# Optimization experiments

Measured on AMD Instinct MI355X. Metric: run time of the kernel, lower is better.

The kernel has to match this reference:

```python
import jax, jax.numpy as jnp
import numpy as np

B, S, D, E, K = 4, 4096, 4096, 64, 8


def setup_inputs() -> dict:
    key = jax.random.key(0)
    k1, k2, k3, k4 = jax.random.split(key, 4)
    scale = 1.0 / np.sqrt(D)
    return {
        "mh_output": jax.random.normal(k1, (B, S, D), dtype=jnp.float32),
        "W_route": jax.random.normal(k2, (E, D), dtype=jnp.float32) * scale,
        "b_route": jnp.zeros((E,), dtype=jnp.float32),
        "W_noise": jax.random.normal(k3, (E, D), dtype=jnp.float32) * scale,
        "b_noise": jnp.zeros((E,), dtype=jnp.float32),
        "noise_eps": jax.random.normal(k4, (B, S, E), dtype=jnp.float32),
        "top_k": K,
    }


def reference(mh_output, W_route, b_route, W_noise, b_noise, noise_eps, top_k):
    # two skinny GEMMs: [B,S,D] x [D,E] -> [B,S,E]
    logits = jnp.einsum("bsd,ed->bse", mh_output, W_route) + b_route
    noise_logits = jnp.einsum("bsd,ed->bse", mh_output, W_noise) + b_noise
    noisy_logits = logits + noise_eps * jax.nn.softplus(noise_logits)
    # top-k selection per token over the expert dim
    _, indices = jax.lax.top_k(noisy_logits, top_k)  # [B,S,K]
    # scatter top-k logits into a -inf tensor == mask non-topk entries
    mask = jnp.any(jax.nn.one_hot(indices, noisy_logits.shape[-1], dtype=jnp.bool_), axis=-2)  # [B,S,E]
    sparse_logits = jnp.where(mask, noisy_logits, -jnp.inf)
    router_output = jax.nn.softmax(sparse_logits, axis=-1)
    return router_output, indices
```

## Files before the change

### kernel.cpp

```cpp
#include <hip/hip_runtime.h>
#include <math.h>

#define D_DIM 4096
#define E_DIM 64
#define KTOP 8
#define TAU 2e-4f
#define BM 64
#define NTS 64
#define STB 49152
#define NST 3

#define WS_LIST 1024
#define WS_IMG 66560
#define WS_Z   (WS_IMG + 2097152)

typedef __attribute__((ext_vector_type(8))) short bf16x8;
typedef __attribute__((ext_vector_type(4))) float f32x4;

#define MFMA(a, b, c) __builtin_amdgcn_mfma_f32_16x16x32_bf16(a, b, c, 0, 0, 0)

typedef const __attribute__((address_space(1))) void gas_void;
typedef __attribute__((address_space(3))) void las_void;
#define GLL16(src, dst) \
    __builtin_amdgcn_global_load_lds((gas_void*)(src), (las_void*)(dst), 16, 0, 0)
#define SCHED_FENCE() __builtin_amdgcn_sched_barrier(0)

__device__ inline void split8(float4 p, float4 q, bf16x8& h8, bf16x8& l8) {
    float xx[8] = {p.x, p.y, p.z, p.w, q.x, q.y, q.z, q.w};
    union { unsigned int w[4]; bf16x8 v; } H, L;
    #pragma unroll
    for (int i = 0; i < 4; ++i) {
        float a = xx[2 * i], b = xx[2 * i + 1];
        unsigned int hw;
        asm("v_cvt_pk_bf16_f32 %0, %1, %2" : "=v"(hw) : "v"(a), "v"(b));
        float ha = __uint_as_float(hw << 16);
        float hb = __uint_as_float(hw & 0xFFFF0000u);
        float ra = a - ha, rb = b - hb;
        unsigned int lw;
        asm("v_cvt_pk_bf16_f32 %0, %1, %2" : "=v"(lw) : "v"(ra), "v"(rb));
        H.w[i] = hw; L.w[i] = lw;
    }
    h8 = H.v; l8 = L.v;
}

__global__ __launch_bounds__(256)
void preconv(const float* __restrict__ Wr, const float* __restrict__ Wn,
             unsigned short* __restrict__ img, unsigned int* __restrict__ cnt)
{
    if (blockIdx.x == 0 && threadIdx.x == 0) *cnt = 0u;
    int t = blockIdx.x * 256 + threadIdx.x;
    int kt = t >> 9, rem = t & 511;
    int koff = rem >> 7, col = rem & 127;
    int k = kt * 32 + koff * 8;
    const float* base = (col < E_DIM) ? (Wr + (size_t)col * D_DIM)
                                      : (Wn + (size_t)(col - E_DIM) * D_DIM);
    float4 x0 = *(const float4*)(base + k);
    float4 x1 = *(const float4*)(base + k + 4);
    bf16x8 h8, l8;
    split8(x0, x1, h8, l8);
    size_t o = (size_t)kt * 8192 + koff * 1024 + col * 8;
    *(bf16x8*)(img + o) = h8;
    *(bf16x8*)(img + o + 4096) = l8;
}

__global__ __launch_bounds__(512)
void gemm_k(const float* __restrict__ mh,
            const unsigned short* __restrict__ Wimg,
            float* __restrict__ zbuf)
{
    extern __shared__ char smem[];

    const int tid  = threadIdx.x;
    const int lane = tid & 63;
    const int wv   = tid >> 6;
    const int wr   = wv >> 1;
    const int wc   = wv & 1;
    const int tok0 = blockIdx.x * BM;
    const int rloc = lane & 15;
    const int koff = lane >> 4;
    const int row  = wr * 16 + rloc;
    const int rsw  = row & 15;

    int boff[4];
    #pragma unroll
    for (int fc = 0; fc < 4; ++fc)
        boff[fc] = koff * 1024 + (wc * 64 + fc * 16 + rloc) * 8;

    const int4* gimg = (const int4*)Wimg;

    const int a_tok = tid >> 4;
    const int a_kq  = (tid & 15) ^ (a_tok & 15);
    const float* asrc0 = mh + (size_t)(tok0 + a_tok) * D_DIM + a_kq * 4;
    const float* asrc1 = mh + (size_t)(tok0 + a_tok + 32) * D_DIM + a_kq * 4;

    f32x4 acc[4];
    #pragma unroll
    for (int fc = 0; fc < 4; ++fc) acc[fc] = {0.f, 0.f, 0.f, 0.f};

    auto stage_issue = [&](int t) {
        char* sb = smem + (t % NST) * STB;
        const int4* gB = gimg + (size_t)t * 2048 + tid;
        int4* dB = (int4*)sb + tid;
        GLL16(gB, dB);
        GLL16(gB + 512,  dB + 512);
        GLL16(gB + 1024, dB + 1024);
        GLL16(gB + 1536, dB + 1536);
        int4* dA = (int4*)(sb + 32768) + tid;
        GLL16(asrc0 + t * 64, dA);
        GLL16(asrc1 + t * 64, dA + 512);
    };

    stage_issue(0);
    SCHED_FENCE();
    stage_issue(1);
    SCHED_FENCE();
    asm volatile("s_waitcnt vmcnt(6)" ::: "memory");
    SCHED_FENCE();
    __builtin_amdgcn_s_barrier();
    SCHED_FENCE();

    for (int kt = 0; kt < NTS; ++kt) {
        if (kt + 2 < NTS) stage_issue(kt + 2);
        SCHED_FENCE();
        {
            const char* sb = smem + (kt % NST) * STB;
            const unsigned short* Bst = (const unsigned short*)sb;
            const char* sa = sb + 32768;
            #pragma unroll
            for (int s = 0; s < 2; ++s) {
                const int kf = s * 8 + 2 * koff;
                float4 f0 = *(const float4*)(sa + (row * 16 + ((kf)     ^ rsw)) * 16);
                float4 f1 = *(const float4*)(sa + (row * 16 + ((kf + 1) ^ rsw)) * 16);
                bf16x8 ah, al;
                split8(f0, f1, ah, al);
                const unsigned short* bb = Bst + s * 8192;
                #pragma unroll
                for (int fc = 0; fc < 4; ++fc) {
                    bf16x8 bh = *(const bf16x8*)(bb + boff[fc]);
                    bf16x8 bl = *(const bf16x8*)(bb + 4096 + boff[fc]);
                    acc[fc] = MFMA(ah, bh, acc[fc]);
                    acc[fc] = MFMA(al, bh, acc[fc]);
                    acc[fc] = MFMA(ah, bl, acc[fc]);
                }
            }
        }
        SCHED_FENCE();
        if (kt + 2 < NTS) {
            asm volatile("s_waitcnt vmcnt(6) lgkmcnt(0)" ::: "memory");
        } else {
            asm volatile("s_waitcnt vmcnt(0) lgkmcnt(0)" ::: "memory");
        }
        SCHED_FENCE();
        __builtin_amdgcn_s_barrier();
        SCHED_FENCE();
    }

    float* zb = zbuf + (size_t)tok0 * 128;
    #pragma unroll
    for (int fc = 0; fc < 4; ++fc) {
        const int col = wc * 64 + fc * 16 + rloc;
        #pragma unroll
        for (int rg = 0; rg < 4; ++rg) {
            const int r = wr * 16 + koff * 4 + rg;
            zb[r * 128 + col] = acc[fc][rg];
        }
    }
}

__global__ __launch_bounds__(256)
void epi_k(const float* __restrict__ zbuf,
           const float* __restrict__ br, const float* __restrict__ bn,
           const float* __restrict__ eps,
           float* __restrict__ out_probs, float* __restrict__ out_idx,
           unsigned int* __restrict__ cnt, int* __restrict__ list)
{
    __shared__ float zs[32 * 132];
    const int tid  = threadIdx.x;
    const int lane = tid & 63;
    const int wv   = tid >> 6;
    const int tok0 = blockIdx.x * 32;

    for (int i = tid; i < 1024; i += 256) {
        int t = i >> 5, q = i & 31;
        float4 v = *(const float4*)(zbuf + (size_t)(tok0 + t) * 128 + q * 4);
        int b = t * 132 + q * 4;
        zs[b] = v.x; zs[b + 1] = v.y; zs[b + 2] = v.z; zs[b + 3] = v.w;
    }
    __syncthreads();

    {
        const int t  = tid >> 3;
        const int e0 = (tid & 7) << 3;
        const float* ep = eps + (size_t)(tok0 + t) * E_DIM + e0;
        #pragma unroll
        for (int j = 0; j < 8; ++j) {
            float zr = zs[t * 132 + e0 + j] + br[e0 + j];
            float zn = zs[t * 132 + 64 + e0 + j] + bn[e0 + j];
            float sp = fmaxf(zn, 0.f) + log1pf(expf(-fabsf(zn)));
            zs[t * 132 + e0 + j] = zr + ep[j] * sp;
        }
    }
    __syncthreads();

    for (int tk = 0; tk < 8; ++tk) {
        int t = wv * 8 + tk;
        float v0 = zs[t * 132 + lane];
        float v  = v0;
        float m0 = 0.f, denom = 0.f, prev = 0.f, mingap = INFINITY;
        bool selected = false;
        int rankedIdx = 0;
        #pragma unroll
        for (int k = 0; k < KTOP + 1; ++k) {
            float mv = v; int mi = lane;
            #pragma unroll
            for (int off = 32; off > 0; off >>= 1) {
                float ov = __shfl_xor(mv, off);
                int   oi = __shfl_xor(mi, off);
                if (ov > mv || (ov == mv && oi < mi)) { mv = ov; mi = oi; }
            }
            if (k == 0) m0 = mv; else mingap = fminf(mingap, prev - mv);
            prev = mv;
            if (k < KTOP) {
                denom += expf(mv - m0);
                if (lane == mi) { selected = true; v = -INFINITY; }
                if (lane == k) rankedIdx = mi;
            }
        }
        float p = selected ? expf(v0 - m0) / denom : 0.f;
        size_t tg = (size_t)(tok0 + t);
        out_probs[tg * E_DIM + lane] = p;
        if (lane < KTOP) out_idx[tg * KTOP + lane] = (float)rankedIdx;
        if (mingap < TAU && lane == 0) {
            unsigned int wpos = atomicAdd(cnt, 1u);
            list[wpos] = (int)tg;
        }
    }
}

__global__ __launch_bounds__(256)
void refine_fp64(const float* __restrict__ mh,
                 const float* __restrict__ Wr, const float* __restrict__ br,
                 const float* __restrict__ Wn, const float* __restrict__ bn,
                 const float* __restrict__ eps,
                 float* __restrict__ out_probs, float* __restrict__ out_idx,
                 const unsigned int* __restrict__ cnt, const int* __restrict__ list)
{
    __shared__ double red[128];
    const unsigned int n = *cnt;
    const int tid  = threadIdx.x;
    const int lane = tid & 63;
    const int wv   = tid >> 6;

    for (unsigned int i = blockIdx.x; i < n; i += gridDim.x) {
        const int tok = list[i];
        const float* xb = mh + (size_t)tok * D_DIM;

        for (int r = 0; r < 32; ++r) {
            const int rrow = wv * 32 + r;
            const float* wp = (rrow < E_DIM) ? (Wr + (size_t)rrow * D_DIM)
                                             : (Wn + (size_t)(rrow - E_DIM) * D_DIM);
            double s0 = 0.0, s1 = 0.0, s2 = 0.0, s3 = 0.0;
            #pragma unroll 4
            for (int k = lane * 4; k < D_DIM; k += 256) {
                float4 xv = *(const float4*)(xb + k);
                float4 w4 = *(const float4*)(wp + k);
                s0 += (double)xv.x * (double)w4.x;
                s1 += (double)xv.y * (double)w4.y;
                s2 += (double)xv.z * (double)w4.z;
                s3 += (double)xv.w * (double)w4.w;
            }
            double s = (s0 + s1) + (s2 + s3);
            #pragma unroll
            for (int off = 32; off > 0; off >>= 1) s += __shfl_xor(s, off);
            if (lane == 0) red[rrow] = s;
        }
        __syncthreads();

        if (wv == 0) {
            double zr = red[lane] + (double)br[lane];
            double zn = red[E_DIM + lane] + (double)bn[lane];
            double sp = fmax(zn, 0.0) + log1p(exp(-fabs(zn)));
            double nl = zr + (double)eps[(size_t)tok * E_DIM + lane] * sp;
            double v = nl, m0 = 0.0, denom = 0.0;
            bool selected = false;
            int rankedIdx = 0;
            #pragma unroll
            for (int k = 0; k < KTOP; ++k) {
                double mv = v; int mi = lane;
                #pragma unroll
                for (int off = 32; off > 0; off >>= 1) {
                    double ov = __shfl_xor(mv, off);
                    int    oi = __shfl_xor(mi, off);
                    if (ov > mv || (ov == mv && oi < mi)) { mv = ov; mi = oi; }
                }
                if (k == 0) m0 = mv;
                denom += exp(mv - m0);
                if (lane == mi) { selected = true; v = -INFINITY; }
                if (lane == k) rankedIdx = mi;
            }
            float p = selected ? (float)(exp(nl - m0) / denom) : 0.f;
            out_probs[(size_t)tok * E_DIM + lane] = p;
            if (lane < KTOP) out_idx[(size_t)tok * KTOP + lane] = (float)rankedIdx;
        }
        __syncthreads();
    }
}

extern "C" void kernel_launch(void* const* d_in, const int* in_sizes, int n_in,
                              void* d_out, int out_size, void* d_ws, size_t ws_size,
                              hipStream_t stream) {
    const float* mh  = (const float*)d_in[0];
    const float* Wr  = (const float*)d_in[1];
    const float* br  = (const float*)d_in[2];
    const float* Wn  = (const float*)d_in[3];
    const float* bn  = (const float*)d_in[4];
    const float* eps = (const float*)d_in[5];

    const int ntok = in_sizes[0] / D_DIM;
    float* out_probs = (float*)d_out;
    float* out_idx   = (float*)d_out + (size_t)ntok * E_DIM;

    unsigned int* cnt = (unsigned int*)d_ws;
    int* list = (int*)((char*)d_ws + WS_LIST);
    unsigned short* img = (unsigned short*)((char*)d_ws + WS_IMG);
    float* zbuf = (float*)((char*)d_ws + WS_Z);

    hipLaunchKernelGGL(preconv, dim3(256), dim3(256), 0, stream, Wr, Wn, img, cnt);
    hipLaunchKernelGGL(gemm_k, dim3(ntok / BM), dim3(512), NST * STB, stream,
                       mh, img, zbuf);
    hipLaunchKernelGGL(epi_k, dim3(ntok / 32), dim3(256), 0, stream,
                       zbuf, br, bn, eps, out_probs, out_idx, cnt, list);
    hipLaunchKernelGGL(refine_fp64, dim3(1024), dim3(256), 0, stream,
                       mh, Wr, br, Wn, bn, eps, out_probs, out_idx, cnt, list);
}
```

Before: 215.6 us.

## Halve GEMM token tile with double buffering and rewrite epilogue as per-thread insertion sort

The GEMM now uses 32-token tiles, 256 threads and two LDS stages instead of three. This doubles the number of blocks and cuts shared memory per block, so the skinny GEMM should fill the device better, at the cost of a shallower prefetch pipeline with full vmcnt(0) waits. The epilogue becomes one thread per token that keeps a top-9 list in registers by insertion, replacing the per-rank wave-wide shuffle reductions. It then stages the probabilities through LDS for coalesced stores. The insertion uses a strict '>' comparison, so on ties the earlier index is kept, which matches the old tie-break.

```diff
diff --git a/kernel.cpp b/kernel.cpp
--- a/kernel.cpp
+++ b/kernel.cpp
@@ -5,10 +5,10 @@
 #define E_DIM 64
 #define KTOP 8
 #define TAU 2e-4f
-#define BM 64
+#define BM 32
 #define NTS 64
-#define STB 49152
-#define NST 3
+#define STB 40960
+#define NST 2
 
 #define WS_LIST 1024
 #define WS_IMG 66560
@@ -63,7 +63,7 @@
     *(bf16x8*)(img + o + 4096) = l8;
 }
 
-__global__ __launch_bounds__(512)
+__global__ __launch_bounds__(256)
 void gemm_k(const float* __restrict__ mh,
             const unsigned short* __restrict__ Wimg,
             float* __restrict__ zbuf)
@@ -91,39 +91,41 @@
     const int a_tok = tid >> 4;
     const int a_kq  = (tid & 15) ^ (a_tok & 15);
     const float* asrc0 = mh + (size_t)(tok0 + a_tok) * D_DIM + a_kq * 4;
-    const float* asrc1 = mh + (size_t)(tok0 + a_tok + 32) * D_DIM + a_kq * 4;
+    const float* asrc1 = mh + (size_t)(tok0 + a_tok + 16) * D_DIM + a_kq * 4;
 
     f32x4 acc[4];
     #pragma unroll
     for (int fc = 0; fc < 4; ++fc) acc[fc] = {0.f, 0.f, 0.f, 0.f};
 
     auto stage_issue = [&](int t) {
-        char* sb = smem + (t % NST) * STB;
+        char* sb = smem + (t & 1) * STB;
         const int4* gB = gimg + (size_t)t * 2048 + tid;
         int4* dB = (int4*)sb + tid;
         GLL16(gB, dB);
+        GLL16(gB + 256,  dB + 256);
         GLL16(gB + 512,  dB + 512);
+        GLL16(gB + 768,  dB + 768);
         GLL16(gB + 1024, dB + 1024);
+        GLL16(gB + 1280, dB + 1280);
         GLL16(gB + 1536, dB + 1536);
+        GLL16(gB + 1792, dB + 1792);
         int4* dA = (int4*)(sb + 32768) + tid;
         GLL16(asrc0 + t * 64, dA);
-        GLL16(asrc1 + t * 64, dA + 512);
+        GLL16(asrc1 + t * 64, dA + 256);
     };
 
     stage_issue(0);
     SCHED_FENCE();
-    stage_issue(1);
-    SCHED_FENCE();
-    asm volatile("s_waitcnt vmcnt(6)" ::: "memory");
+    asm volatile("s_waitcnt vmcnt(0)" ::: "memory");
     SCHED_FENCE();
     __builtin_amdgcn_s_barrier();
     SCHED_FENCE();
 
     for (int kt = 0; kt < NTS; ++kt) {
-        if (kt + 2 < NTS) stage_issue(kt + 2);
+        if (kt + 1 < NTS) stage_issue(kt + 1);
         SCHED_FENCE();
         {
-            const char* sb = smem + (kt % NST) * STB;
+            const char* sb = smem + (kt & 1) * STB;
             const unsigned short* Bst = (const unsigned short*)sb;
             const char* sa = sb + 32768;
             #pragma unroll
@@ -145,11 +147,7 @@
             }
         }
         SCHED_FENCE();
-        if (kt + 2 < NTS) {
-            asm volatile("s_waitcnt vmcnt(6) lgkmcnt(0)" ::: "memory");
-        } else {
-            asm volatile("s_waitcnt vmcnt(0) lgkmcnt(0)" ::: "memory");
-        }
+        asm volatile("s_waitcnt vmcnt(0) lgkmcnt(0)" ::: "memory");
         SCHED_FENCE();
         __builtin_amdgcn_s_barrier();
         SCHED_FENCE();
@@ -167,70 +165,84 @@
     }
 }
 
-__global__ __launch_bounds__(256)
+#define ISTEP(K) { bool gt = cv > v##K; \
+    float tv = gt ? cv : v##K; int ti = gt ? ci : j##K; \
+    float sv = gt ? v##K : cv; int si = gt ? j##K : ci; \
+    v##K = tv; j##K = ti; cv = sv; ci = si; }
+
+__global__ __launch_bounds__(64)
 void epi_k(const float* __restrict__ zbuf,
            const float* __restrict__ br, const float* __restrict__ bn,
            const float* __restrict__ eps,
            float* __restrict__ out_probs, float* __restrict__ out_idx,
            unsigned int* __restrict__ cnt, int* __restrict__ list)
 {
-    __shared__ float zs[32 * 132];
+    __shared__ float ns[64 * 65];
+    __shared__ float ps[64 * 65];
     const int tid  = threadIdx.x;
-    const int lane = tid & 63;
-    const int wv   = tid >> 6;
-    const int tok0 = blockIdx.x * 32;
-
-    for (int i = tid; i < 1024; i += 256) {
-        int t = i >> 5, q = i & 31;
-        float4 v = *(const float4*)(zbuf + (size_t)(tok0 + t) * 128 + q * 4);
-        int b = t * 132 + q * 4;
-        zs[b] = v.x; zs[b + 1] = v.y; zs[b + 2] = v.z; zs[b + 3] = v.w;
+    const int tok0 = blockIdx.x * 64;
+
+    for (int i = tid; i < 1024; i += 64) {
+        const int t = i >> 4, q = i & 15;
+        const float* zb = zbuf + (size_t)(tok0 + t) * 128 + q * 4;
+        float4 zr4 = *(const float4*)zb;
+        float4 zn4 = *(const float4*)(zb + 64);
+        float4 ep4 = *(const float4*)(eps + (size_t)(tok0 + t) * E_DIM + q * 4);
+        float4 br4 = *(const float4*)(br + q * 4);
+        float4 bn4 = *(const float4*)(bn + q * 4);
+        float zr[4] = {zr4.x, zr4.y, zr4.z, zr4.w};
+        float zn[4] = {zn4.x, zn4.y, zn4.z, zn4.w};
+        float ep[4] = {ep4.x, ep4.y, ep4.z, ep4.w};
+        float bb[4] = {br4.x, br4.y, br4.z, br4.w};
+        float cc[4] = {bn4.x, bn4.y, bn4.z, bn4.w};
+        #pragma unroll
+        for (int j = 0; j < 4; ++j) {
+            float n = zn[j] + cc[j];
+            float sp = fmaxf(n, 0.f) + log1pf(expf(-fabsf(n)));
+            ns[t * 65 + q * 4 + j] = (zr[j] + bb[j]) + ep[j] * sp;
+        }
     }
     __syncthreads();
 
+    float v0 = -INFINITY, v1 = -INFINITY, v2 = -INFINITY, v3 = -INFINITY,
+          v4 = -INFINITY, v5 = -INFINITY, v6 = -INFINITY, v7 = -INFINITY,
+          v8 = -INFINITY;
+    int j0 = 0, j1 = 0, j2 = 0, j3 = 0, j4 = 0, j5 = 0, j6 = 0, j7 = 0, j8 = 0;
+    const float* nrow = ns + tid * 65;
+    for (int e = 0; e < 64; ++e) {
+        float cv = nrow[e]; int ci = e;
+        ISTEP(0) ISTEP(1) ISTEP(2) ISTEP(3) ISTEP(4)
+        ISTEP(5) ISTEP(6) ISTEP(7) ISTEP(8)
+    }
+    const float m0 = v0;
+    float denom = expf(v0 - m0) + expf(v1 - m0) + expf(v2 - m0) + expf(v3 - m0)
+                + expf(v4 - m0) + expf(v5 - m0) + expf(v6 - m0) + expf(v7 - m0);
+    float mingap = fminf(fminf(fminf(v0 - v1, v1 - v2), fminf(v2 - v3, v3 - v4)),
+                         fminf(fminf(v4 - v5, v5 - v6), fminf(v6 - v7, v7 - v8)));
+
+    float* prow = ps + tid * 65;
+    #pragma unroll 8
+    for (int e = 0; e < 64; ++e) prow[e] = 0.f;
+    prow[j0] = expf(v0 - m0) / denom;
+    prow[j1] = expf(v1 - m0) / denom;
+    prow[j2] = expf(v2 - m0) / denom;
+    prow[j3] = expf(v3 - m0) / denom;
+    prow[j4] = expf(v4 - m0) / denom;
+    prow[j5] = expf(v5 - m0) / denom;
+    prow[j6] = expf(v6 - m0) / denom;
+    prow[j7] = expf(v7 - m0) / denom;
+    __syncthreads();
+
+    for (int i = tid; i < 4096; i += 64) {
+        const int t = i >> 6, e = i & 63;
+        out_probs[(size_t)(tok0 + t) * E_DIM + e] = ps[t * 65 + e];
+    }
     {
-        const int t  = tid >> 3;
-        const int e0 = (tid & 7) << 3;
-        const float* ep = eps + (size_t)(tok0 + t) * E_DIM + e0;
-        #pragma unroll
-        for (int j = 0; j < 8; ++j) {
-            float zr = zs[t * 132 + e0 + j] + br[e0 + j];
-            float zn = zs[t * 132 + 64 + e0 + j] + bn[e0 + j];
-            float sp = fmaxf(zn, 0.f) + log1pf(expf(-fabsf(zn)));
-            zs[t * 132 + e0 + j] = zr + ep[j] * sp;
-        }
-    }
-    __syncthreads();
-
-    for (int tk = 0; tk < 8; ++tk) {
-        int t = wv * 8 + tk;
-        float v0 = zs[t * 132 + lane];
-        float v  = v0;
-        float m0 = 0.f, denom = 0.f, prev = 0.f, mingap = INFINITY;
-        bool selected = false;
-        int rankedIdx = 0;
-        #pragma unroll
-        for (int k = 0; k < KTOP + 1; ++k) {
-            float mv = v; int mi = lane;
-            #pragma unroll
-            for (int off = 32; off > 0; off >>= 1) {
-                float ov = __shfl_xor(mv, off);
-                int   oi = __shfl_xor(mi, off);
-                if (ov > mv || (ov == mv && oi < mi)) { mv = ov; mi = oi; }
-            }
-            if (k == 0) m0 = mv; else mingap = fminf(mingap, prev - mv);
-            prev = mv;
-            if (k < KTOP) {
-                denom += expf(mv - m0);
-                if (lane == mi) { selected = true; v = -INFINITY; }
-                if (lane == k) rankedIdx = mi;
-            }
-        }
-        float p = selected ? expf(v0 - m0) / denom : 0.f;
-        size_t tg = (size_t)(tok0 + t);
-        out_probs[tg * E_DIM + lane] = p;
-        if (lane < KTOP) out_idx[tg * KTOP + lane] = (float)rankedIdx;
-        if (mingap < TAU && lane == 0) {
+        const size_t tg = (size_t)(tok0 + tid);
+        float* oi = out_idx + tg * KTOP;
+        oi[0] = (float)j0; oi[1] = (float)j1; oi[2] = (float)j2; oi[3] = (float)j3;
+        oi[4] = (float)j4; oi[5] = (float)j5; oi[6] = (float)j6; oi[7] = (float)j7;
+        if (mingap < TAU) {
             unsigned int wpos = atomicAdd(cnt, 1u);
             list[wpos] = (int)tg;
         }
@@ -326,9 +338,9 @@
     float* zbuf = (float*)((char*)d_ws + WS_Z);
 
     hipLaunchKernelGGL(preconv, dim3(256), dim3(256), 0, stream, Wr, Wn, img, cnt);
-    hipLaunchKernelGGL(gemm_k, dim3(ntok / BM), dim3(512), NST * STB, stream,
+    hipLaunchKernelGGL(gemm_k, dim3(ntok / BM), dim3(256), NST * STB, stream,
                        mh, img, zbuf);
-    hipLaunchKernelGGL(epi_k, dim3(ntok / 32), dim3(256), 0, stream,
+    hipLaunchKernelGGL(epi_k, dim3(ntok / 64), dim3(64), 0, stream,
                        zbuf, br, bn, eps, out_probs, out_idx, cnt, list);
     hipLaunchKernelGGL(refine_fp64, dim3(1024), dim3(256), 0, stream,
                        mh, Wr, br, Wn, bn, eps, out_probs, out_idx, cnt, list);
```

Result: faster. 190.3 us (-11.7%).
